# Kernel optimization log

Hardware: AMD Instinct MI355X
Metric: run time of the kernel (lower is better)

## Reference

```python
import jax, jax.numpy as jnp
import numpy as np

HIDDEN = 4096
Q_HEADS = 32
KV_HEADS = 8
HEAD_DIM = 128
MAX_LEN = 8192
PAST_LEN = 4096
SEQ_LEN = 16
BSZ = 1
REPEAT_KV = Q_HEADS // KV_HEADS
SCALE = HEAD_DIM ** (-0.5)


def _apply_rope(x):
    # x: [b, h, s, d]; positions start at 0 (faithful to source, even for cached k)
    s, d = x.shape[2], x.shape[3]
    half = d // 2
    positions = jnp.arange(s, dtype=x.dtype)
    inv_freq = jnp.arange(half, dtype=x.dtype) / half
    angles = positions[:, None] * inv_freq[None, :]          # [s, half]
    sin = jnp.sin(angles)[None, None]
    cos = jnp.cos(angles)[None, None]
    x_even, x_odd = x[..., :half], x[..., half:]
    return jnp.concatenate([x_even * cos - x_odd * sin,
                            x_even * sin + x_odd * cos], axis=-1)


def setup_inputs() -> dict:
    key = jax.random.key(0)
    ks = jax.random.split(key, 5)
    qkv_dim = (Q_HEADS + 2 * KV_HEADS) * HEAD_DIM
    x = jax.random.normal(ks[0], (BSZ, SEQ_LEN, HIDDEN), dtype=jnp.float32)
    w_qkv = jax.random.normal(ks[1], (qkv_dim, HIDDEN), dtype=jnp.float32) * 0.02
    w_out = jax.random.normal(ks[2], (HIDDEN, Q_HEADS * HEAD_DIM), dtype=jnp.float32) * 0.02
    cache_k = jax.random.normal(ks[3], (1, KV_HEADS, MAX_LEN, HEAD_DIM), dtype=jnp.float32)
    cache_v = jax.random.normal(ks[4], (1, KV_HEADS, MAX_LEN, HEAD_DIM), dtype=jnp.float32)
    return {"x": x, "w_qkv": w_qkv, "w_out": w_out, "cache_k": cache_k, "cache_v": cache_v}


def reference(x, w_qkv, w_out, cache_k, cache_v):
    bsz, seq_len, _ = x.shape
    qkv = jnp.einsum('bsh,oh->bso', x, w_qkv)
    q_size = Q_HEADS * HEAD_DIM
    kv_size = KV_HEADS * HEAD_DIM
    q = qkv[..., :q_size].reshape(bsz, seq_len, Q_HEADS, HEAD_DIM).transpose(0, 2, 1, 3)
    k = qkv[..., q_size:q_size + kv_size].reshape(bsz, seq_len, KV_HEADS, HEAD_DIM).transpose(0, 2, 1, 3)
    v = qkv[..., q_size + kv_size:].reshape(bsz, seq_len, KV_HEADS, HEAD_DIM).transpose(0, 2, 1, 3)
    q = _apply_rope(q)
    k = _apply_rope(k)
    # KV-cache append (static slice positions)
    cache_k = cache_k.at[:, :, PAST_LEN:PAST_LEN + seq_len, :].set(k)
    cache_v = cache_v.at[:, :, PAST_LEN:PAST_LEN + seq_len, :].set(v)
    key_len = PAST_LEN + seq_len
    key = cache_k[:, :, :key_len, :]
    value = cache_v[:, :, :key_len, :]
    if REPEAT_KV > 1:  # GQA broadcast
        key = jnp.repeat(key, REPEAT_KV, axis=1)
        value = jnp.repeat(value, REPEAT_KV, axis=1)
    scores = jnp.einsum('bhqd,bhkd->bhqk', q, key) * SCALE
    q_pos = jnp.arange(seq_len)
    k_pos = jnp.arange(key_len)
    mask = (k_pos[None, :] <= q_pos[:, None] + PAST_LEN).astype(scores.dtype)
    scores = scores + (1.0 - mask)[None, None] * -10000.0
    weights = jax.nn.softmax(scores, axis=-1)
    out = jnp.einsum('bhqk,bhkd->bhqd', weights, value)
    out = out.transpose(0, 2, 1, 3).reshape(bsz, seq_len, Q_HEADS * HEAD_DIM)
    return jnp.einsum('bso,ho->bsh', out, w_out)
```

## Files before the change

kernel.cpp:

```cpp
#include <hip/hip_runtime.h>
#include <hip/hip_bf16.h>

typedef __bf16 bf16;
typedef __bf16 bf16x8 __attribute__((ext_vector_type(8)));
typedef float f32x4 __attribute__((ext_vector_type(4)));

#define HID 4096
#define QKVN 6144
#define NQH 32
#define NKVH 8
#define HD 128
#define MAXLEN 8192
#define PAST 4096
#define SQ 16
#define NC 33
#define CHUNK 128
#define SCALE 0.08838834764831845f
#define NEGBIG (-30000.0f)

__device__ __forceinline__ f32x4 mfma16(bf16x8 a, bf16x8 b, f32x4 c) {
  return __builtin_amdgcn_mfma_f32_16x16x32_bf16(a, b, c, 0, 0, 0);
}

__device__ __forceinline__ bf16x8 load8f(const float* p) {
  const f32x4* q = (const f32x4*)p;
  f32x4 a = q[0], b = q[1];
  bf16x8 r;
  r[0] = (bf16)a[0]; r[1] = (bf16)a[1]; r[2] = (bf16)a[2]; r[3] = (bf16)a[3];
  r[4] = (bf16)b[0]; r[5] = (bf16)b[1]; r[6] = (bf16)b[2]; r[7] = (bf16)b[3];
  return r;
}

__global__ __launch_bounds__(256) void qkv_kernel(const float* __restrict__ x,
                                                  const float* __restrict__ wq,
                                                  float* __restrict__ qkv_acc) {
  int tid = threadIdx.x, lane = tid & 63, wv = tid >> 6;
  int l15 = lane & 15, quad = lane >> 4;
  int n = blockIdx.x * 16 + l15;
  const float* wrow = wq + (size_t)n * HID + quad * 8;
  const float* xrow = x + (size_t)l15 * HID + quad * 8;
  f32x4 acc = {0.f, 0.f, 0.f, 0.f};
  int kbeg = wv * (HID / 4);
#pragma unroll 8
  for (int k = 0; k < HID / 4; k += 32) {
    bf16x8 a = load8f(xrow + kbeg + k);
    bf16x8 b = load8f(wrow + kbeg + k);
    acc = mfma16(a, b, acc);
  }
  __shared__ __align__(16) float red[4][64][4];
  *(f32x4*)(&red[wv][lane][0]) = acc;
  __syncthreads();
  if (wv == 0) {
#pragma unroll
    for (int r = 0; r < 4; ++r) {
      float v = red[0][lane][r] + red[1][lane][r] + red[2][lane][r] + red[3][lane][r];
      qkv_acc[(quad * 4 + r) * QKVN + blockIdx.x * 16 + l15] = v;
    }
  }
}

template <bool NEW>
__device__ void attn_body(int kvh, int c,
                          const float* __restrict__ ck, const float* __restrict__ cv,
                          const float* __restrict__ qkv_acc,
                          bf16* __restrict__ Opart, float* __restrict__ ml,
                          bf16* Vt, bf16* Pl) {
  int tid = threadIdx.x, lane = tid & 63, wv = tid >> 6;
  int l15 = lane & 15, quad = lane >> 4;
  int qh = kvh * 4 + wv;
  int cs = c * CHUNK;

  if (!NEW) {
    int key = tid & 127;
    int dr = (tid >> 7) * 64;
    const float* vrow = cv + ((size_t)kvh * MAXLEN + cs + key) * HD + dr;
#pragma unroll
    for (int mb = 0; mb < 8; ++mb) {
      bf16x8 v = load8f(vrow + mb * 8);
#pragma unroll
      for (int i = 0; i < 8; ++i) Vt[(dr + mb * 8 + i) * 136 + key] = v[i];
    }
  } else {
    int key = tid & 15;
    int dr = (tid >> 4) * 8;
    const float* vsrc = qkv_acc + (size_t)key * QKVN + (PAST + NKVH * HD) + kvh * HD + dr;
#pragma unroll
    for (int i = 0; i < 8; ++i) {
      Vt[(dr + i) * 136 + key] = (bf16)vsrc[i];
      Vt[(dr + i) * 136 + 16 + key] = (bf16)0.f;
    }
  }
  __syncthreads();

  bf16x8 afrag[4];
  {
    const float* qrow = qkv_acc + (size_t)l15 * QKVN + qh * HD;
    float fm = (float)l15;
#pragma unroll
    for (int kk = 0; kk < 4; ++kk) {
      bf16x8 a;
#pragma unroll
      for (int j = 0; j < 8; ++j) {
        int d = kk * 32 + quad * 8 + j;
        int dh = d & 63;
        float ang = fm * (float)dh * (1.0f / 64.0f);
        float sn, co;
        __sincosf(ang, &sn, &co);
        float qe = qrow[dh], qo = qrow[dh + 64];
        float v = (d < 64) ? (qe * co - qo * sn) : (qe * sn + qo * co);
        a[j] = (bf16)(v * SCALE);
      }
      afrag[kk] = a;
    }
  }

  constexpr int NT = NEW ? 1 : 8;
  f32x4 sc[NT];
  if (!NEW) {
#pragma unroll
    for (int nt = 0; nt < NT; ++nt) {
      const float* krow = ck + ((size_t)kvh * MAXLEN + cs + nt * 16 + l15) * HD + quad * 8;
      f32x4 acc = {0.f, 0.f, 0.f, 0.f};
#pragma unroll
      for (int kk = 0; kk < 4; ++kk)
        acc = mfma16(afrag[kk], load8f(krow + kk * 32), acc);
      sc[nt] = acc;
    }
  } else {
    const float* krow = qkv_acc + (size_t)l15 * QKVN + PAST + kvh * HD;
    float ft = (float)l15;
    f32x4 acc = {0.f, 0.f, 0.f, 0.f};
#pragma unroll
    for (int kk = 0; kk < 4; ++kk) {
      bf16x8 b;
#pragma unroll
      for (int j = 0; j < 8; ++j) {
        int d = kk * 32 + quad * 8 + j;
        int dh = d & 63;
        float ang = ft * (float)dh * (1.0f / 64.0f);
        float sn, co;
        __sincosf(ang, &sn, &co);
        float ke = krow[dh], ko = krow[dh + 64];
        b[j] = (bf16)((d < 64) ? (ke * co - ko * sn) : (ke * sn + ko * co));
      }
      acc = mfma16(afrag[kk], b, acc);
    }
#pragma unroll
    for (int r = 0; r < 4; ++r)
      if (l15 > quad * 4 + r) acc[r] = NEGBIG;
    sc[0] = acc;
  }

  float mx[4], sm[4];
#pragma unroll
  for (int r = 0; r < 4; ++r) {
    float v = sc[0][r];
#pragma unroll
    for (int nt = 1; nt < NT; ++nt) v = fmaxf(v, sc[nt][r]);
    v = fmaxf(v, __shfl_xor(v, 1));
    v = fmaxf(v, __shfl_xor(v, 2));
    v = fmaxf(v, __shfl_xor(v, 4));
    v = fmaxf(v, __shfl_xor(v, 8));
    mx[r] = v;
  }
#pragma unroll
  for (int nt = 0; nt < NT; ++nt)
#pragma unroll
    for (int r = 0; r < 4; ++r) sc[nt][r] = __expf(sc[nt][r] - mx[r]);
#pragma unroll
  for (int r = 0; r < 4; ++r) {
    float v = 0.f;
#pragma unroll
    for (int nt = 0; nt < NT; ++nt) v += sc[nt][r];
    v += __shfl_xor(v, 1);
    v += __shfl_xor(v, 2);
    v += __shfl_xor(v, 4);
    v += __shfl_xor(v, 8);
    sm[r] = v;
  }

  bf16* Pw = Pl + wv * 16 * 136;
#pragma unroll
  for (int nt = 0; nt < NT; ++nt)
#pragma unroll
    for (int r = 0; r < 4; ++r)
      Pw[(quad * 4 + r) * 136 + nt * 16 + l15] = (bf16)sc[nt][r];
  if (NEW) {
#pragma unroll
    for (int r = 0; r < 4; ++r)
      Pw[(quad * 4 + r) * 136 + 16 + l15] = (bf16)0.f;
  }
  __syncthreads();

  constexpr int KI = NEW ? 1 : 4;
  int prow = ((kvh * NC + c) * 4 + wv) * 16;
  bf16* ob = Opart + (size_t)prow * 128;
#pragma unroll
  for (int nt2 = 0; nt2 < 8; ++nt2) {
    f32x4 acc = {0.f, 0.f, 0.f, 0.f};
#pragma unroll
    for (int kk = 0; kk < KI; ++kk) {
      bf16x8 a = *(const bf16x8*)(Pw + l15 * 136 + kk * 32 + quad * 8);
      bf16x8 b = *(const bf16x8*)(Vt + (nt2 * 16 + l15) * 136 + kk * 32 + quad * 8);
      acc = mfma16(a, b, acc);
    }
#pragma unroll
    for (int r = 0; r < 4; ++r)
      ob[(quad * 4 + r) * 128 + nt2 * 16 + l15] = (bf16)acc[r];
  }
  if (l15 == 0) {
#pragma unroll
    for (int r = 0; r < 4; ++r) {
      ml[(size_t)(prow + quad * 4 + r) * 2] = mx[r];
      ml[(size_t)(prow + quad * 4 + r) * 2 + 1] = sm[r];
    }
  }
}

__global__ __launch_bounds__(256) void attn_kernel(const float* __restrict__ ck,
                                                   const float* __restrict__ cv,
                                                   const float* __restrict__ qkv_acc,
                                                   bf16* __restrict__ Opart,
                                                   float* __restrict__ ml) {
  __shared__ __align__(16) bf16 VtLds[128 * 136];
  __shared__ __align__(16) bf16 PLds[4 * 16 * 136];
  int c = blockIdx.x % NC;
  int kvh = blockIdx.x / NC;
  if (c == NC - 1)
    attn_body<true>(kvh, c, ck, cv, qkv_acc, Opart, ml, VtLds, PLds);
  else
    attn_body<false>(kvh, c, ck, cv, qkv_acc, Opart, ml, VtLds, PLds);
}

__global__ __launch_bounds__(256) void combine_kernel(const bf16* __restrict__ Opart,
                                                      const float* __restrict__ ml,
                                                      bf16* __restrict__ attn_out) {
  int tid = threadIdx.x, lane = tid & 63, wv = tid >> 6;
  int gw = blockIdx.x * 4 + wv;
  int qh = gw >> 4, srow = gw & 15;
  int kvh = qh >> 2, lw = qh & 3;
  int rowbase = ((kvh * NC) * 4 + lw) * 16 + srow;
  const float* mlb = ml + (size_t)rowbase * 2;
  float m_c = NEGBIG, l_c = 0.f;
  if (lane < NC) {
    m_c = mlb[(size_t)lane * 128];
    l_c = mlb[(size_t)lane * 128 + 1];
  }
  float M = m_c;
  M = fmaxf(M, __shfl_xor(M, 1));
  M = fmaxf(M, __shfl_xor(M, 2));
  M = fmaxf(M, __shfl_xor(M, 4));
  M = fmaxf(M, __shfl_xor(M, 8));
  M = fmaxf(M, __shfl_xor(M, 16));
  M = fmaxf(M, __shfl_xor(M, 32));
  float w = (lane < NC) ? __expf(m_c - M) : 0.f;
  float Lp = w * l_c;
  Lp += __shfl_xor(Lp, 1);
  Lp += __shfl_xor(Lp, 2);
  Lp += __shfl_xor(Lp, 4);
  Lp += __shfl_xor(Lp, 8);
  Lp += __shfl_xor(Lp, 16);
  Lp += __shfl_xor(Lp, 32);
  float a0 = 0.f, a1 = 0.f;
  const bf16* ob = Opart + (size_t)rowbase * 128;
  for (int cc = 0; cc < NC; ++cc) {
    float wc = __shfl(w, cc);
    const bf16* oc = ob + (size_t)cc * 64 * 128;
    a0 += wc * (float)oc[lane];
    a1 += wc * (float)oc[64 + lane];
  }
  float inv = 1.f / Lp;
  attn_out[srow * HID + qh * HD + lane] = (bf16)(a0 * inv);
  attn_out[srow * HID + qh * HD + 64 + lane] = (bf16)(a1 * inv);
}

__global__ __launch_bounds__(256) void proj_kernel(const bf16* __restrict__ attn_out,
                                                   const float* __restrict__ wo,
                                                   float* __restrict__ out) {
  int tid = threadIdx.x, lane = tid & 63, wv = tid >> 6;
  int l15 = lane & 15, quad = lane >> 4;
  int n = blockIdx.x * 16 + l15;
  const float* wrow = wo + (size_t)n * HID + quad * 8;
  const bf16* arow = attn_out + (size_t)l15 * HID + quad * 8;
  f32x4 acc = {0.f, 0.f, 0.f, 0.f};
  int kbeg = wv * (HID / 4);
#pragma unroll 8
  for (int k = 0; k < HID / 4; k += 32) {
    bf16x8 a = *(const bf16x8*)(arow + kbeg + k);
    bf16x8 b = load8f(wrow + kbeg + k);
    acc = mfma16(a, b, acc);
  }
  __shared__ __align__(16) float red[4][64][4];
  *(f32x4*)(&red[wv][lane][0]) = acc;
  __syncthreads();
  if (wv == 0) {
#pragma unroll
    for (int r = 0; r < 4; ++r) {
      float v = red[0][lane][r] + red[1][lane][r] + red[2][lane][r] + red[3][lane][r];
      out[(quad * 4 + r) * HID + blockIdx.x * 16 + l15] = v;
    }
  }
}

extern "C" void kernel_launch(void* const* d_in, const int* in_sizes, int n_in,
                              void* d_out, int out_size, void* d_ws, size_t ws_size,
                              hipStream_t stream) {
  const float* x       = (const float*)d_in[0];
  const float* w_qkv   = (const float*)d_in[1];
  const float* w_out   = (const float*)d_in[2];
  const float* cache_k = (const float*)d_in[3];
  const float* cache_v = (const float*)d_in[4];
  float* out = (float*)d_out;

  float* qkv_acc = (float*)d_ws;
  float* ml = qkv_acc + SQ * QKVN;
  bf16* attn_out = (bf16*)(ml + (size_t)NKVH * NC * 4 * 16 * 2);
  bf16* Opart = attn_out + (size_t)SQ * HID;

  hipLaunchKernelGGL(qkv_kernel, dim3(QKVN / 16), dim3(256), 0, stream, x, w_qkv, qkv_acc);
  hipLaunchKernelGGL(attn_kernel, dim3(NKVH * NC), dim3(256), 0, stream, cache_k, cache_v, qkv_acc, Opart, ml);
  hipLaunchKernelGGL(combine_kernel, dim3(128), dim3(256), 0, stream, Opart, ml, attn_out);
  hipLaunchKernelGGL(proj_kernel, dim3(HID / 16), dim3(256), 0, stream, attn_out, w_out, out);
}
```

Baseline: 287.2 us.

## Split-K GEMMs with LDS-staged weights, precomputed RoPE Q/K, smaller attention chunks

Replaces the QKV and output projections with a split-K GEMM (8 K-slices, 3072 and 2048 blocks) that stages coalesced fp32 weight rows into LDS as bf16, and adds separate reduction kernels. RoPE, scaling and the bf16 fragment layout for Q/K/V move into a finish kernel, so the attention kernel no longer recomputes sincos. Attention chunks shrink to 64 keys (520 blocks), with K staged through LDS via coalesced loads, and combine is adapted to 65 chunks. The aim is more memory-level parallelism for the bandwidth-bound weight and cache reads, at the cost of extra launches and partial-sum traffic.

```diff
diff --git a/kernel.cpp b/kernel.cpp
--- a/kernel.cpp
+++ b/kernel.cpp
@@ -2,6 +2,7 @@
 #include <hip/hip_bf16.h>
 
 typedef __bf16 bf16;
+typedef __bf16 bf16x4 __attribute__((ext_vector_type(4)));
 typedef __bf16 bf16x8 __attribute__((ext_vector_type(8)));
 typedef float f32x4 __attribute__((ext_vector_type(4)));
 
@@ -13,10 +14,14 @@
 #define MAXLEN 8192
 #define PAST 4096
 #define SQ 16
-#define NC 33
-#define CHUNK 128
 #define SCALE 0.08838834764831845f
 #define NEGBIG (-30000.0f)
+
+#define KS 8
+#define KPB 512
+#define WSTR 520
+#define ACH 64
+#define NCH 65
 
 __device__ __forceinline__ f32x4 mfma16(bf16x8 a, bf16x8 b, f32x4 c) {
   return __builtin_amdgcn_mfma_f32_16x16x32_bf16(a, b, c, 0, 0, 0);
@@ -31,119 +36,180 @@
   return r;
 }
 
-__global__ __launch_bounds__(256) void qkv_kernel(const float* __restrict__ x,
-                                                  const float* __restrict__ wq,
-                                                  float* __restrict__ qkv_acc) {
+__device__ __forceinline__ int fmidx(int k, int m) {
+  return ((k >> 3) * 16 + m) * 8 + (k & 7);
+}
+
+__global__ __launch_bounds__(256) void xprep_kernel(const float* __restrict__ x,
+                                                    bf16* __restrict__ xf) {
+  int id = blockIdx.x * 256 + threadIdx.x;
+  int m = id & 15, o = id >> 4;
+  bf16x8 v = load8f(x + (size_t)m * HID + o * 8);
+  *(bf16x8*)(xf + (size_t)(o * 16 + m) * 8) = v;
+}
+
+template <int NT>
+__global__ __launch_bounds__(256) void gemm16_kernel(const bf16* __restrict__ afrag,
+                                                     const float* __restrict__ w,
+                                                     float* __restrict__ partial) {
   int tid = threadIdx.x, lane = tid & 63, wv = tid >> 6;
   int l15 = lane & 15, quad = lane >> 4;
-  int n = blockIdx.x * 16 + l15;
-  const float* wrow = wq + (size_t)n * HID + quad * 8;
-  const float* xrow = x + (size_t)l15 * HID + quad * 8;
+  int nt = blockIdx.x % NT, kq = blockIdx.x / NT;
+
+  __shared__ __align__(16) bf16 Wt[16 * WSTR];
+  __shared__ __align__(16) float red[4][64][4];
+
+  const float* wb = w + (size_t)(nt * 16) * HID + kq * KPB;
+  int r2 = tid >> 7;
+  int c4 = tid & 127;
+  f32x4 stg[8];
+#pragma unroll
+  for (int it = 0; it < 8; ++it)
+    stg[it] = *(const f32x4*)(wb + (size_t)(it * 2 + r2) * HID + c4 * 4);
+
+  int obase = kq * 64 + wv * 16;
+  bf16x8 af[4];
+#pragma unroll
+  for (int kk = 0; kk < 4; ++kk)
+    af[kk] = *(const bf16x8*)(afrag + (size_t)((obase + kk * 4 + quad) * 16 + l15) * 8);
+
+#pragma unroll
+  for (int it = 0; it < 8; ++it) {
+    bf16x4 t;
+    t[0] = (bf16)stg[it][0]; t[1] = (bf16)stg[it][1];
+    t[2] = (bf16)stg[it][2]; t[3] = (bf16)stg[it][3];
+    *(bf16x4*)(Wt + (it * 2 + r2) * WSTR + c4 * 4) = t;
+  }
+  __syncthreads();
+
   f32x4 acc = {0.f, 0.f, 0.f, 0.f};
-  int kbeg = wv * (HID / 4);
-#pragma unroll 8
-  for (int k = 0; k < HID / 4; k += 32) {
-    bf16x8 a = load8f(xrow + kbeg + k);
-    bf16x8 b = load8f(wrow + kbeg + k);
-    acc = mfma16(a, b, acc);
-  }
-  __shared__ __align__(16) float red[4][64][4];
+#pragma unroll
+  for (int kk = 0; kk < 4; ++kk) {
+    bf16x8 b = *(const bf16x8*)(Wt + l15 * WSTR + wv * 128 + kk * 32 + quad * 8);
+    acc = mfma16(af[kk], b, acc);
+  }
+
   *(f32x4*)(&red[wv][lane][0]) = acc;
   __syncthreads();
   if (wv == 0) {
 #pragma unroll
     for (int r = 0; r < 4; ++r) {
       float v = red[0][lane][r] + red[1][lane][r] + red[2][lane][r] + red[3][lane][r];
-      qkv_acc[(quad * 4 + r) * QKVN + blockIdx.x * 16 + l15] = v;
-    }
+      partial[((size_t)(kq * NT + nt) * 16 + (quad * 4 + r)) * 16 + l15] = v;
+    }
+  }
+}
+
+__device__ __forceinline__ float sum_part(const float* p, int NT, int n, int m) {
+  float s = 0.f;
+#pragma unroll
+  for (int q = 0; q < KS; ++q)
+    s += p[((size_t)(q * NT + (n >> 4)) * 16 + m) * 16 + (n & 15)];
+  return s;
+}
+
+__global__ __launch_bounds__(256) void qkv_finish_kernel(const float* __restrict__ pq,
+                                                         bf16* __restrict__ Qf,
+                                                         bf16* __restrict__ Kf,
+                                                         bf16* __restrict__ Vn) {
+  int id = blockIdx.x * 256 + threadIdx.x;
+  if (id < 32768) {
+    int qh = id >> 10, m = (id >> 6) & 15, j = id & 63;
+    float e = sum_part(pq, 384, qh * 128 + j, m);
+    float o = sum_part(pq, 384, qh * 128 + 64 + j, m);
+    float sn, co;
+    __sincosf((float)m * (float)j * (1.0f / 64.0f), &sn, &co);
+    Qf[qh * 2048 + fmidx(j, m)] = (bf16)((e * co - o * sn) * SCALE);
+    Qf[qh * 2048 + fmidx(j + 64, m)] = (bf16)((e * sn + o * co) * SCALE);
+  } else if (id < 40960) {
+    int v = id - 32768;
+    int kvh = v >> 10, m = (v >> 6) & 15, j = v & 63;
+    float e = sum_part(pq, 384, 4096 + kvh * 128 + j, m);
+    float o = sum_part(pq, 384, 4096 + kvh * 128 + 64 + j, m);
+    float sn, co;
+    __sincosf((float)m * (float)j * (1.0f / 64.0f), &sn, &co);
+    Kf[kvh * 2048 + fmidx(j, m)] = (bf16)(e * co - o * sn);
+    Kf[kvh * 2048 + fmidx(j + 64, m)] = (bf16)(e * sn + o * co);
+  } else if (id < 57344) {
+    int v = id - 40960;
+    int kvh = v >> 11, m = (v >> 7) & 15, d = v & 127;
+    Vn[kvh * 2048 + m * 128 + d] = (bf16)sum_part(pq, 384, 5120 + kvh * 128 + d, m);
   }
 }
 
 template <bool NEW>
 __device__ void attn_body(int kvh, int c,
                           const float* __restrict__ ck, const float* __restrict__ cv,
-                          const float* __restrict__ qkv_acc,
+                          const bf16* __restrict__ Qf, const bf16* __restrict__ Kf,
+                          const bf16* __restrict__ Vn,
                           bf16* __restrict__ Opart, float* __restrict__ ml,
-                          bf16* Vt, bf16* Pl) {
+                          bf16* Kt, bf16* Vt, bf16* Pl) {
   int tid = threadIdx.x, lane = tid & 63, wv = tid >> 6;
   int l15 = lane & 15, quad = lane >> 4;
   int qh = kvh * 4 + wv;
-  int cs = c * CHUNK;
+  int cs = c * ACH;
 
   if (!NEW) {
-    int key = tid & 127;
-    int dr = (tid >> 7) * 64;
-    const float* vrow = cv + ((size_t)kvh * MAXLEN + cs + key) * HD + dr;
-#pragma unroll
-    for (int mb = 0; mb < 8; ++mb) {
-      bf16x8 v = load8f(vrow + mb * 8);
-#pragma unroll
-      for (int i = 0; i < 8; ++i) Vt[(dr + mb * 8 + i) * 136 + key] = v[i];
+    {
+      int kr = tid >> 5;
+      int kc4 = tid & 31;
+      f32x4 kst[8];
+#pragma unroll
+      for (int it = 0; it < 8; ++it)
+        kst[it] = *(const f32x4*)(ck + ((size_t)(kvh * MAXLEN + cs + it * 8 + kr)) * HD + kc4 * 4);
+      int key = tid & 63, dg = tid >> 6;
+      f32x4 vst[8];
+#pragma unroll
+      for (int q4 = 0; q4 < 8; ++q4)
+        vst[q4] = *(const f32x4*)(cv + ((size_t)(kvh * MAXLEN + cs + key)) * HD + dg * 32 + q4 * 4);
+#pragma unroll
+      for (int it = 0; it < 8; ++it) {
+        bf16x4 t;
+        t[0] = (bf16)kst[it][0]; t[1] = (bf16)kst[it][1];
+        t[2] = (bf16)kst[it][2]; t[3] = (bf16)kst[it][3];
+        *(bf16x4*)(Kt + (it * 8 + kr) * 136 + kc4 * 4) = t;
+      }
+#pragma unroll
+      for (int q4 = 0; q4 < 8; ++q4)
+#pragma unroll
+        for (int i = 0; i < 4; ++i)
+          Vt[(dg * 32 + q4 * 4 + i) * 72 + key] = (bf16)vst[q4][i];
     }
   } else {
-    int key = tid & 15;
-    int dr = (tid >> 4) * 8;
-    const float* vsrc = qkv_acc + (size_t)key * QKVN + (PAST + NKVH * HD) + kvh * HD + dr;
+    int key = tid >> 4, dg8 = tid & 15;
+    bf16x8 v = *(const bf16x8*)(Vn + kvh * 2048 + key * 128 + dg8 * 8);
 #pragma unroll
     for (int i = 0; i < 8; ++i) {
-      Vt[(dr + i) * 136 + key] = (bf16)vsrc[i];
-      Vt[(dr + i) * 136 + 16 + key] = (bf16)0.f;
+      Vt[(dg8 * 8 + i) * 72 + key] = v[i];
+      Vt[(dg8 * 8 + i) * 72 + 16 + key] = (bf16)0.f;
     }
   }
   __syncthreads();
 
-  bf16x8 afrag[4];
-  {
-    const float* qrow = qkv_acc + (size_t)l15 * QKVN + qh * HD;
-    float fm = (float)l15;
-#pragma unroll
-    for (int kk = 0; kk < 4; ++kk) {
-      bf16x8 a;
-#pragma unroll
-      for (int j = 0; j < 8; ++j) {
-        int d = kk * 32 + quad * 8 + j;
-        int dh = d & 63;
-        float ang = fm * (float)dh * (1.0f / 64.0f);
-        float sn, co;
-        __sincosf(ang, &sn, &co);
-        float qe = qrow[dh], qo = qrow[dh + 64];
-        float v = (d < 64) ? (qe * co - qo * sn) : (qe * sn + qo * co);
-        a[j] = (bf16)(v * SCALE);
-      }
-      afrag[kk] = a;
-    }
-  }
-
-  constexpr int NT = NEW ? 1 : 8;
+  bf16x8 af[4];
+#pragma unroll
+  for (int kk = 0; kk < 4; ++kk)
+    af[kk] = *(const bf16x8*)(Qf + qh * 2048 + ((kk * 4 + quad) * 16 + l15) * 8);
+
+  constexpr int NT = NEW ? 1 : 4;
   f32x4 sc[NT];
   if (!NEW) {
 #pragma unroll
     for (int nt = 0; nt < NT; ++nt) {
-      const float* krow = ck + ((size_t)kvh * MAXLEN + cs + nt * 16 + l15) * HD + quad * 8;
       f32x4 acc = {0.f, 0.f, 0.f, 0.f};
 #pragma unroll
-      for (int kk = 0; kk < 4; ++kk)
-        acc = mfma16(afrag[kk], load8f(krow + kk * 32), acc);
+      for (int kk = 0; kk < 4; ++kk) {
+        bf16x8 b = *(const bf16x8*)(Kt + (nt * 16 + l15) * 136 + kk * 32 + quad * 8);
+        acc = mfma16(af[kk], b, acc);
+      }
       sc[nt] = acc;
     }
   } else {
-    const float* krow = qkv_acc + (size_t)l15 * QKVN + PAST + kvh * HD;
-    float ft = (float)l15;
     f32x4 acc = {0.f, 0.f, 0.f, 0.f};
 #pragma unroll
     for (int kk = 0; kk < 4; ++kk) {
-      bf16x8 b;
-#pragma unroll
-      for (int j = 0; j < 8; ++j) {
-        int d = kk * 32 + quad * 8 + j;
-        int dh = d & 63;
-        float ang = ft * (float)dh * (1.0f / 64.0f);
-        float sn, co;
-        __sincosf(ang, &sn, &co);
-        float ke = krow[dh], ko = krow[dh + 64];
-        b[j] = (bf16)((d < 64) ? (ke * co - ko * sn) : (ke * sn + ko * co));
-      }
-      acc = mfma16(afrag[kk], b, acc);
+      bf16x8 b = *(const bf16x8*)(Kf + kvh * 2048 + ((kk * 4 + quad) * 16 + l15) * 8);
+      acc = mfma16(af[kk], b, acc);
     }
 #pragma unroll
     for (int r = 0; r < 4; ++r)
@@ -179,29 +245,29 @@
     sm[r] = v;
   }
 
-  bf16* Pw = Pl + wv * 16 * 136;
+  bf16* Pw = Pl + wv * 16 * 72;
 #pragma unroll
   for (int nt = 0; nt < NT; ++nt)
 #pragma unroll
     for (int r = 0; r < 4; ++r)
-      Pw[(quad * 4 + r) * 136 + nt * 16 + l15] = (bf16)sc[nt][r];
+      Pw[(quad * 4 + r) * 72 + nt * 16 + l15] = (bf16)sc[nt][r];
   if (NEW) {
 #pragma unroll
     for (int r = 0; r < 4; ++r)
-      Pw[(quad * 4 + r) * 136 + 16 + l15] = (bf16)0.f;
+      Pw[(quad * 4 + r) * 72 + 16 + l15] = (bf16)0.f;
   }
   __syncthreads();
 
-  constexpr int KI = NEW ? 1 : 4;
-  int prow = ((kvh * NC + c) * 4 + wv) * 16;
-  bf16* ob = Opart + (size_t)prow * 128;
+  constexpr int KI = NEW ? 1 : 2;
+  int rowblk = ((kvh * NCH + c) * 4 + wv) * 16;
+  bf16* ob = Opart + (size_t)rowblk * 128;
 #pragma unroll
   for (int nt2 = 0; nt2 < 8; ++nt2) {
     f32x4 acc = {0.f, 0.f, 0.f, 0.f};
 #pragma unroll
     for (int kk = 0; kk < KI; ++kk) {
-      bf16x8 a = *(const bf16x8*)(Pw + l15 * 136 + kk * 32 + quad * 8);
-      bf16x8 b = *(const bf16x8*)(Vt + (nt2 * 16 + l15) * 136 + kk * 32 + quad * 8);
+      bf16x8 a = *(const bf16x8*)(Pw + l15 * 72 + kk * 32 + quad * 8);
+      bf16x8 b = *(const bf16x8*)(Vt + (nt2 * 16 + l15) * 72 + kk * 32 + quad * 8);
       acc = mfma16(a, b, acc);
     }
 #pragma unroll
@@ -211,50 +277,56 @@
   if (l15 == 0) {
 #pragma unroll
     for (int r = 0; r < 4; ++r) {
-      ml[(size_t)(prow + quad * 4 + r) * 2] = mx[r];
-      ml[(size_t)(prow + quad * 4 + r) * 2 + 1] = sm[r];
+      ml[(size_t)(rowblk + quad * 4 + r) * 2] = mx[r];
+      ml[(size_t)(rowblk + quad * 4 + r) * 2 + 1] = sm[r];
     }
   }
 }
 
 __global__ __launch_bounds__(256) void attn_kernel(const float* __restrict__ ck,
                                                    const float* __restrict__ cv,
-                                                   const float* __restrict__ qkv_acc,
+                                                   const bf16* __restrict__ Qf,
+                                                   const bf16* __restrict__ Kf,
+                                                   const bf16* __restrict__ Vn,
                                                    bf16* __restrict__ Opart,
                                                    float* __restrict__ ml) {
-  __shared__ __align__(16) bf16 VtLds[128 * 136];
-  __shared__ __align__(16) bf16 PLds[4 * 16 * 136];
-  int c = blockIdx.x % NC;
-  int kvh = blockIdx.x / NC;
-  if (c == NC - 1)
-    attn_body<true>(kvh, c, ck, cv, qkv_acc, Opart, ml, VtLds, PLds);
+  __shared__ __align__(16) bf16 KtL[64 * 136];
+  __shared__ __align__(16) bf16 VtL[128 * 72];
+  __shared__ __align__(16) bf16 PL[4 * 16 * 72];
+  int c = blockIdx.x % NCH;
+  int kvh = blockIdx.x / NCH;
+  if (c == NCH - 1)
+    attn_body<true>(kvh, c, ck, cv, Qf, Kf, Vn, Opart, ml, KtL, VtL, PL);
   else
-    attn_body<false>(kvh, c, ck, cv, qkv_acc, Opart, ml, VtLds, PLds);
+    attn_body<false>(kvh, c, ck, cv, Qf, Kf, Vn, Opart, ml, KtL, VtL, PL);
 }
 
 __global__ __launch_bounds__(256) void combine_kernel(const bf16* __restrict__ Opart,
                                                       const float* __restrict__ ml,
-                                                      bf16* __restrict__ attn_out) {
+                                                      bf16* __restrict__ attfm) {
   int tid = threadIdx.x, lane = tid & 63, wv = tid >> 6;
   int gw = blockIdx.x * 4 + wv;
   int qh = gw >> 4, srow = gw & 15;
   int kvh = qh >> 2, lw = qh & 3;
-  int rowbase = ((kvh * NC) * 4 + lw) * 16 + srow;
-  const float* mlb = ml + (size_t)rowbase * 2;
-  float m_c = NEGBIG, l_c = 0.f;
-  if (lane < NC) {
-    m_c = mlb[(size_t)lane * 128];
-    l_c = mlb[(size_t)lane * 128 + 1];
-  }
-  float M = m_c;
+  int rowblk0 = ((kvh * NCH) * 4 + lw) * 16 + srow;
+  const float* mlb = ml + (size_t)rowblk0 * 2;
+  float m1 = mlb[(size_t)lane * 128];
+  float l1 = mlb[(size_t)lane * 128 + 1];
+  float m2 = NEGBIG, l2 = 0.f;
+  if (lane == 0) {
+    m2 = mlb[(size_t)64 * 128];
+    l2 = mlb[(size_t)64 * 128 + 1];
+  }
+  float M = fmaxf(m1, m2);
   M = fmaxf(M, __shfl_xor(M, 1));
   M = fmaxf(M, __shfl_xor(M, 2));
   M = fmaxf(M, __shfl_xor(M, 4));
   M = fmaxf(M, __shfl_xor(M, 8));
   M = fmaxf(M, __shfl_xor(M, 16));
   M = fmaxf(M, __shfl_xor(M, 32));
-  float w = (lane < NC) ? __expf(m_c - M) : 0.f;
-  float Lp = w * l_c;
+  float w1 = __expf(m1 - M);
+  float w2 = (lane == 0) ? __expf(m2 - M) : 0.f;
+  float Lp = w1 * l1 + w2 * l2;
   Lp += __shfl_xor(Lp, 1);
   Lp += __shfl_xor(Lp, 2);
   Lp += __shfl_xor(Lp, 4);
@@ -262,44 +334,34 @@
   Lp += __shfl_xor(Lp, 16);
   Lp += __shfl_xor(Lp, 32);
   float a0 = 0.f, a1 = 0.f;
-  const bf16* ob = Opart + (size_t)rowbase * 128;
-  for (int cc = 0; cc < NC; ++cc) {
-    float wc = __shfl(w, cc);
-    const bf16* oc = ob + (size_t)cc * 64 * 128;
+  const bf16* ob = Opart + (size_t)rowblk0 * 128;
+  for (int cc = 0; cc < 64; ++cc) {
+    float wc = __shfl(w1, cc);
+    const bf16* oc = ob + (size_t)cc * 8192;
     a0 += wc * (float)oc[lane];
     a1 += wc * (float)oc[64 + lane];
   }
+  {
+    float wc = __shfl(w2, 0);
+    const bf16* oc = ob + (size_t)64 * 8192;
+    a0 += wc * (float)oc[lane];
+    a1 += wc * (float)oc[64 + lane];
+  }
   float inv = 1.f / Lp;
-  attn_out[srow * HID + qh * HD + lane] = (bf16)(a0 * inv);
-  attn_out[srow * HID + qh * HD + 64 + lane] = (bf16)(a1 * inv);
-}
-
-__global__ __launch_bounds__(256) void proj_kernel(const bf16* __restrict__ attn_out,
-                                                   const float* __restrict__ wo,
-                                                   float* __restrict__ out) {
-  int tid = threadIdx.x, lane = tid & 63, wv = tid >> 6;
-  int l15 = lane & 15, quad = lane >> 4;
-  int n = blockIdx.x * 16 + l15;
-  const float* wrow = wo + (size_t)n * HID + quad * 8;
-  const bf16* arow = attn_out + (size_t)l15 * HID + quad * 8;
-  f32x4 acc = {0.f, 0.f, 0.f, 0.f};
-  int kbeg = wv * (HID / 4);
-#pragma unroll 8
-  for (int k = 0; k < HID / 4; k += 32) {
-    bf16x8 a = *(const bf16x8*)(arow + kbeg + k);
-    bf16x8 b = load8f(wrow + kbeg + k);
-    acc = mfma16(a, b, acc);
-  }
-  __shared__ __align__(16) float red[4][64][4];
-  *(f32x4*)(&red[wv][lane][0]) = acc;
-  __syncthreads();
-  if (wv == 0) {
-#pragma unroll
-    for (int r = 0; r < 4; ++r) {
-      float v = red[0][lane][r] + red[1][lane][r] + red[2][lane][r] + red[3][lane][r];
-      out[(quad * 4 + r) * HID + blockIdx.x * 16 + l15] = v;
-    }
-  }
+  int k1 = qh * 128 + lane, k2 = k1 + 64;
+  attfm[fmidx(k1, srow)] = (bf16)(a0 * inv);
+  attfm[fmidx(k2, srow)] = (bf16)(a1 * inv);
+}
+
+__global__ __launch_bounds__(256) void proj_reduce_kernel(const float* __restrict__ pp,
+                                                          float* __restrict__ out) {
+  int flat = blockIdx.x * 256 + threadIdx.x;
+  int m = flat >> 10, n = (flat & 1023) * 4;
+  f32x4 s = {0.f, 0.f, 0.f, 0.f};
+#pragma unroll
+  for (int q = 0; q < KS; ++q)
+    s += *(const f32x4*)(pp + ((size_t)(q * 256 + (n >> 4)) * 16 + m) * 16 + (n & 15));
+  *(f32x4*)(out + (size_t)m * HID + n) = s;
 }
 
 extern "C" void kernel_launch(void* const* d_in, const int* in_sizes, int n_in,
@@ -312,13 +374,23 @@
   const float* cache_v = (const float*)d_in[4];
   float* out = (float*)d_out;
 
-  float* qkv_acc = (float*)d_ws;
-  float* ml = qkv_acc + SQ * QKVN;
-  bf16* attn_out = (bf16*)(ml + (size_t)NKVH * NC * 4 * 16 * 2);
-  bf16* Opart = attn_out + (size_t)SQ * HID;
-
-  hipLaunchKernelGGL(qkv_kernel, dim3(QKVN / 16), dim3(256), 0, stream, x, w_qkv, qkv_acc);
-  hipLaunchKernelGGL(attn_kernel, dim3(NKVH * NC), dim3(256), 0, stream, cache_k, cache_v, qkv_acc, Opart, ml);
-  hipLaunchKernelGGL(combine_kernel, dim3(128), dim3(256), 0, stream, Opart, ml, attn_out);
-  hipLaunchKernelGGL(proj_kernel, dim3(HID / 16), dim3(256), 0, stream, attn_out, w_out, out);
-}
+  char* p = (char*)d_ws;
+  bf16*  Xfrag = (bf16*)p;               p += (size_t)16 * HID * 2;
+  float* partQ = (float*)p;              p += (size_t)KS * 384 * 256 * 4;
+  bf16*  Qf    = (bf16*)p;               p += (size_t)NQH * 2048 * 2;
+  bf16*  Kf    = (bf16*)p;               p += (size_t)NKVH * 2048 * 2;
+  bf16*  Vn    = (bf16*)p;               p += (size_t)NKVH * 2048 * 2;
+  bf16*  Opart = (bf16*)p;               p += (size_t)NKVH * NCH * 4 * 16 * 128 * 2;
+  float* ml    = (float*)p;              p += (size_t)NKVH * NCH * 4 * 16 * 2 * 4;
+  bf16*  attfm = (bf16*)p;               p += (size_t)16 * HID * 2;
+  float* partP = (float*)p;              p += (size_t)KS * 256 * 256 * 4;
+
+  hipLaunchKernelGGL(xprep_kernel, dim3(32), dim3(256), 0, stream, x, Xfrag);
+  hipLaunchKernelGGL((gemm16_kernel<384>), dim3(384 * KS), dim3(256), 0, stream, Xfrag, w_qkv, partQ);
+  hipLaunchKernelGGL(qkv_finish_kernel, dim3(224), dim3(256), 0, stream, partQ, Qf, Kf, Vn);
+  hipLaunchKernelGGL(attn_kernel, dim3(NKVH * NCH), dim3(256), 0, stream,
+                     cache_k, cache_v, Qf, Kf, Vn, Opart, ml);
+  hipLaunchKernelGGL(combine_kernel, dim3(128), dim3(256), 0, stream, Opart, ml, attfm);
+  hipLaunchKernelGGL((gemm16_kernel<256>), dim3(256 * KS), dim3(256), 0, stream, attfm, w_out, partP);
+  hipLaunchKernelGGL(proj_reduce_kernel, dim3(64), dim3(256), 0, stream, partP, out);
+}
```

Result: faster. 255.2 us (-11.1%).
